# Optimization experiments

Measured on AMD Instinct MI355X. Metric: run time of the kernel, lower is better.

## Reference

```python
import jax, jax.numpy as jnp
import numpy as np

B, C, N, K, E = 8, 64, 4096, 16, 64
EPS = 1e-5


def _bn(h, gamma, beta, axes):
    # BatchNorm in training mode: stats over batch+spatial axes, per channel (dim 1)
    m = jnp.mean(h, axis=axes, keepdims=True)
    v = jnp.var(h, axis=axes, keepdims=True)
    shape = (1, -1) + (1,) * (h.ndim - 2)
    return gamma.reshape(shape) * (h - m) * jax.lax.rsqrt(v + EPS) + beta.reshape(shape)


def setup_inputs() -> dict:
    key = jax.random.key(0)
    ks = jax.random.split(key, 8)
    x = jax.random.normal(ks[0], (B, C, N), dtype=jnp.float32)
    idx = jax.random.randint(ks[1], (B, N, K), 0, N, dtype=jnp.int32)
    s1 = 1.0 / np.sqrt(C)
    s2 = 1.0 / np.sqrt(E)
    return {
        "x": x,
        "idx": idx,
        "W1": jax.random.normal(ks[2], (E, C), jnp.float32) * s1,
        "b1": jnp.zeros((E,), jnp.float32),
        "g1": jnp.ones((E,), jnp.float32),
        "be1": jnp.zeros((E,), jnp.float32),
        "W2": jax.random.normal(ks[3], (E, E), jnp.float32) * s2,
        "b2": jnp.zeros((E,), jnp.float32),
        "g2": jnp.ones((E,), jnp.float32),
        "be2": jnp.zeros((E,), jnp.float32),
        "W3": jax.random.normal(ks[4], (E, E), jnp.float32) * s2,
        "b3": jnp.zeros((E,), jnp.float32),
        "g3": jnp.ones((E,), jnp.float32),
        "be3": jnp.zeros((E,), jnp.float32),
    }


def reference(x, idx, W1, b1, g1, be1, W2, b2, g2, be2, W3, b3, g3, be3):
    # gather kNN neighbor features: x[b, :, idx[b]] -> (B, C, N, K)
    nn_feat = jax.vmap(lambda xb, ib: xb[:, ib])(x, idx)
    # edge features: neighbor - center
    h = nn_feat - x[..., None]                                   # (B, C, N, K)
    # Conv2DBlock: two 1x1 conv + BN + ReLU layers
    h = jnp.einsum('bcnk,oc->bonk', h, W1) + b1[:, None, None]
    h = jax.nn.relu(_bn(h, g1, be1, (0, 2, 3)))
    h = jnp.einsum('bcnk,oc->bonk', h, W2) + b2[:, None, None]
    h = jax.nn.relu(_bn(h, g2, be2, (0, 2, 3)))
    # max over neighbors
    h = jnp.max(h, axis=-1)                                      # (B, E, N)
    # Conv1DBlock: 1x1 conv + BN + ReLU
    h = jnp.einsum('bcn,oc->bon', h, W3) + b3[:, None]
    h = jax.nn.relu(_bn(h, g3, be3, (0, 2)))
    return h
```

## Files before the change

kernel.cpp:

```cpp
#include <hip/hip_runtime.h>

#define EPSBN 1e-5f
#define CNT1 524288.0f
#define CNT3 32768.0f
#define NREP 16

typedef short v8s __attribute__((ext_vector_type(8)));
typedef float v16f __attribute__((ext_vector_type(16)));

__device__ __forceinline__ unsigned short f2bf(float f) {
  union { float f; unsigned u; } v; v.f = f;
  unsigned u = v.u;
  u += 0x7fffu + ((u >> 16) & 1u);
  return (unsigned short)(u >> 16);
}
__device__ __forceinline__ unsigned pack2bf(float a, float b) {
  return (unsigned)f2bf(a) | ((unsigned)f2bf(b) << 16);
}
__device__ __forceinline__ float bflo(unsigned u) {
  union { unsigned u; float f; } v; v.u = u << 16; return v.f;
}
__device__ __forceinline__ float bfhi(unsigned u) {
  union { unsigned u; float f; } v; v.u = u & 0xffff0000u; return v.f;
}

__global__ __launch_bounds__(256) void prep(
    const float* __restrict__ x, const float* __restrict__ W1,
    const float* __restrict__ W2, const float* __restrict__ W3,
    unsigned short* __restrict__ y, unsigned short* __restrict__ Wbf) {
  int blk = blockIdx.x, t = threadIdx.x;
  if (blk >= 512) {
    int i = (blk - 512) * 256 + t;
    const float* src = (i < 4096) ? W2 : W3;
    Wbf[i] = f2bf(src[i & 4095]);
    return;
  }
  __shared__ unsigned short ldsX[64 * 72];
  int b = blk >> 6, n0 = (blk & 63) << 6;
  int tn = t & 63, cg = t >> 6;
#pragma unroll
  for (int i = 0; i < 16; ++i) {
    int c = cg * 16 + i;
    ldsX[tn * 72 + c] = f2bf(x[(((size_t)(b * 64 + c)) << 12) + n0 + tn]);
  }
  __syncthreads();
  int lane = t & 63, w = t >> 6;
  int l31 = lane & 31, lh = lane >> 5;
  int ot = w & 1, ph = w >> 1;
  int o = ot * 32 + l31;
  v16f acc;
#pragma unroll
  for (int i = 0; i < 16; ++i) acc[i] = 0.f;
#pragma unroll
  for (int ks = 0; ks < 4; ++ks) {
    const float* wrow = W1 + o * 64 + ks * 16 + lh * 8;
    float4 wa = *((const float4*)wrow);
    float4 wb = *((const float4*)(wrow + 4));
    v8s wf; unsigned* wu = (unsigned*)&wf;
    wu[0] = pack2bf(wa.x, wa.y); wu[1] = pack2bf(wa.z, wa.w);
    wu[2] = pack2bf(wb.x, wb.y); wu[3] = pack2bf(wb.z, wb.w);
    v8s af = *((const v8s*)&ldsX[(ph * 32 + l31) * 72 + ks * 16 + lh * 8]);
    acc = __builtin_amdgcn_mfma_f32_32x32x16_bf16(af, wf, acc, 0, 0, 0);
  }
#pragma unroll
  for (int i = 0; i < 16; ++i) {
    int row = (i & 3) + ((i >> 2) << 3) + (lh << 2);
    int pt = (b << 12) + n0 + ph * 32 + row;
    y[pt * 64 + o] = f2bf(acc[i]);
  }
}

__global__ __launch_bounds__(256) void p1_stats(
    const unsigned short* __restrict__ y, const int* __restrict__ idx,
    float* __restrict__ S1) {
  __shared__ float bs[64], bq[64];
  int t = threadIdx.x;
  if (t < 64) { bs[t] = 0.f; bq[t] = 0.f; }
  __syncthreads();
  int blk = blockIdx.x;
  int batch = blk & 7, bi = blk >> 3;
  int w = t >> 6, lane = t & 63;
  int ch = (lane & 7) << 3, eg = lane >> 3;
  int ebase = (batch << 16) + bi * 512 + w * 128;
  float ss[8], sq[8];
#pragma unroll
  for (int k = 0; k < 8; ++k) { ss[k] = 0.f; sq[k] = 0.f; }
  for (int it = 0; it < 16; ++it) {
    int p = ebase + it * 8 + eg;
    int j = idx[p];
    int site = p >> 4;
    uint4 uj = *((const uint4*)(y + (((size_t)((batch << 12) + j)) << 6) + ch));
    uint4 ui = *((const uint4*)(y + (((size_t)site) << 6) + ch));
    const unsigned* aj = (const unsigned*)&uj;
    const unsigned* ai = (const unsigned*)&ui;
#pragma unroll
    for (int d = 0; d < 4; ++d) {
      float d0 = bflo(aj[d]) - bflo(ai[d]);
      float d1 = bfhi(aj[d]) - bfhi(ai[d]);
      ss[2 * d] += d0; sq[2 * d] += d0 * d0;
      ss[2 * d + 1] += d1; sq[2 * d + 1] += d1 * d1;
    }
  }
#pragma unroll
  for (int k = 0; k < 8; ++k) {
    ss[k] += __shfl_xor(ss[k], 8);  sq[k] += __shfl_xor(sq[k], 8);
    ss[k] += __shfl_xor(ss[k], 16); sq[k] += __shfl_xor(sq[k], 16);
    ss[k] += __shfl_xor(ss[k], 32); sq[k] += __shfl_xor(sq[k], 32);
  }
  if (lane < 8) {
#pragma unroll
    for (int k = 0; k < 8; ++k) {
      atomicAdd(&bs[ch + k], ss[k]);
      atomicAdd(&bq[ch + k], sq[k]);
    }
  }
  __syncthreads();
  int rep = (blk >> 3) & (NREP - 1);
  if (t < 64) atomicAdd(&S1[rep * 128 + t], bs[t]);
  else if (t < 128) atomicAdd(&S1[rep * 128 + t], bq[t - 64]);
}

__global__ __launch_bounds__(256) void p1b_uv(
    const unsigned short* __restrict__ y,
    const float* __restrict__ g1, const float* __restrict__ be1,
    const float* __restrict__ S1,
    unsigned short* __restrict__ u, unsigned short* __restrict__ v) {
  __shared__ float lA[64], lC[64];
  int t = threadIdx.x;
  if (t < 64) {
    float s = 0.f, q = 0.f;
#pragma unroll
    for (int r = 0; r < NREP; ++r) { s += S1[r * 128 + t]; q += S1[r * 128 + 64 + t]; }
    float mean = s / CNT1;
    float var = q / CNT1 - mean * mean;
    float a = g1[t] * rsqrtf(var + EPSBN);
    lA[t] = a; lC[t] = be1[t] - mean * a;
  }
  __syncthreads();
  int pt = blockIdx.x * 64 + (t >> 2);
  int cq = (t & 3) << 4;
  const uint4* yp = (const uint4*)(y + (size_t)pt * 64 + cq);
  uint4 y0 = yp[0], y1 = yp[1];
  uint4 uo[2], vo[2];
  unsigned* up = (unsigned*)uo;
  unsigned* vp = (unsigned*)vo;
#pragma unroll
  for (int d = 0; d < 8; ++d) {
    unsigned yd = (d < 4) ? ((const unsigned*)&y0)[d] : ((const unsigned*)&y1)[d - 4];
    int c = cq + 2 * d;
    float f0 = bflo(yd), f1 = bfhi(yd);
    float a0 = lA[c], a1 = lA[c + 1];
    up[d] = pack2bf(f0 * a0 + lC[c], f1 * a1 + lC[c + 1]);
    vp[d] = pack2bf(f0 * a0, f1 * a1);
  }
  uint4* ud = (uint4*)(u + (size_t)pt * 64 + cq);
  uint4* vd = (uint4*)(v + (size_t)pt * 64 + cq);
  ud[0] = uo[0]; ud[1] = uo[1];
  vd[0] = vo[0]; vd[1] = vo[1];
}

__global__ __launch_bounds__(256) void p2_main(
    const unsigned short* __restrict__ u, const unsigned short* __restrict__ v,
    const int* __restrict__ idx, const unsigned short* __restrict__ Wb,
    unsigned short* __restrict__ mnb, unsigned short* __restrict__ mxb,
    float* __restrict__ S2) {
  __shared__ float bs[64], bq[64];
  int t = threadIdx.x;
  if (t < 64) { bs[t] = 0.f; bq[t] = 0.f; }
  __syncthreads();
  int blk = blockIdx.x;
  int batch = blk & 7, bi = blk >> 3;
  int w = t >> 6, lane = t & 63;
  int l31 = lane & 31, lh = lane >> 5;
  v8s w2[2][4];
#pragma unroll
  for (int s = 0; s < 2; ++s)
#pragma unroll
    for (int ks = 0; ks < 4; ++ks)
      w2[s][ks] = *((const v8s*)(Wb + (s * 32 + l31) * 64 + ks * 16 + lh * 8));
  float ss0 = 0.f, sq0 = 0.f, ss1 = 0.f, sq1 = 0.f;
#pragma unroll
  for (int it = 0; it < 2; ++it) {
    int tile = bi * 8 + w * 2 + it;
    int p = (batch << 16) + (tile << 5) + l31;
    int j = idx[p];
    int site = p >> 4;
    const unsigned short* ur = u + (((size_t)((batch << 12) + j)) << 6) + lh * 8;
    const unsigned short* vr = v + (((size_t)site) << 6) + lh * 8;
    v16f b0, b1;
#pragma unroll
    for (int i = 0; i < 16; ++i) { b0[i] = 0.f; b1[i] = 0.f; }
#pragma unroll
    for (int ks = 0; ks < 4; ++ks) {
      uint4 uu = *((const uint4*)(ur + ks * 16));
      uint4 vv = *((const uint4*)(vr + ks * 16));
      const unsigned* uw = (const unsigned*)&uu;
      const unsigned* vw = (const unsigned*)&vv;
      v8s af; unsigned* au = (unsigned*)&af;
#pragma unroll
      for (int d = 0; d < 4; ++d) {
        float e0 = fmaxf(bflo(uw[d]) - bflo(vw[d]), 0.f);
        float e1 = fmaxf(bfhi(uw[d]) - bfhi(vw[d]), 0.f);
        au[d] = pack2bf(e0, e1);
      }
      b0 = __builtin_amdgcn_mfma_f32_32x32x16_bf16(af, w2[0][ks], b0, 0, 0, 0);
      b1 = __builtin_amdgcn_mfma_f32_32x32x16_bf16(af, w2[1][ks], b1, 0, 0, 0);
    }
    float mx00 = b0[0], mn00 = b0[0], mx01 = b0[8], mn01 = b0[8];
    float mx10 = b1[0], mn10 = b1[0], mx11 = b1[8], mn11 = b1[8];
#pragma unroll
    for (int i = 0; i < 16; ++i) {
      ss0 += b0[i]; sq0 += b0[i] * b0[i];
      ss1 += b1[i]; sq1 += b1[i] * b1[i];
    }
#pragma unroll
    for (int i = 1; i < 8; ++i) {
      mx00 = fmaxf(mx00, b0[i]);     mn00 = fminf(mn00, b0[i]);
      mx01 = fmaxf(mx01, b0[8 + i]); mn01 = fminf(mn01, b0[8 + i]);
      mx10 = fmaxf(mx10, b1[i]);     mn10 = fminf(mn10, b1[i]);
      mx11 = fmaxf(mx11, b1[8 + i]); mn11 = fminf(mn11, b1[8 + i]);
    }
    mx00 = fmaxf(mx00, __shfl_xor(mx00, 32)); mn00 = fminf(mn00, __shfl_xor(mn00, 32));
    mx01 = fmaxf(mx01, __shfl_xor(mx01, 32)); mn01 = fminf(mn01, __shfl_xor(mn01, 32));
    mx10 = fmaxf(mx10, __shfl_xor(mx10, 32)); mn10 = fminf(mn10, __shfl_xor(mn10, 32));
    mx11 = fmaxf(mx11, __shfl_xor(mx11, 32)); mn11 = fminf(mn11, __shfl_xor(mn11, 32));
    int s2 = (batch << 12) + (tile << 1);
    if (lh == 0) {
      mnb[(size_t)(s2 + 0) * 64 + l31] = f2bf(mn00);
      mnb[(size_t)(s2 + 1) * 64 + l31] = f2bf(mn01);
      mnb[(size_t)(s2 + 0) * 64 + 32 + l31] = f2bf(mn10);
      mnb[(size_t)(s2 + 1) * 64 + 32 + l31] = f2bf(mn11);
    } else {
      mxb[(size_t)(s2 + 0) * 64 + l31] = f2bf(mx00);
      mxb[(size_t)(s2 + 1) * 64 + l31] = f2bf(mx01);
      mxb[(size_t)(s2 + 0) * 64 + 32 + l31] = f2bf(mx10);
      mxb[(size_t)(s2 + 1) * 64 + 32 + l31] = f2bf(mx11);
    }
  }
  ss0 += __shfl_xor(ss0, 32); sq0 += __shfl_xor(sq0, 32);
  ss1 += __shfl_xor(ss1, 32); sq1 += __shfl_xor(sq1, 32);
  if (lh == 0) {
    atomicAdd(&bs[l31], ss0); atomicAdd(&bq[l31], sq0);
    atomicAdd(&bs[32 + l31], ss1); atomicAdd(&bq[32 + l31], sq1);
  }
  __syncthreads();
  int rep = blk & (NREP - 1);
  if (t < 64) atomicAdd(&S2[rep * 128 + t], bs[t]);
  else if (t < 128) atomicAdd(&S2[rep * 128 + t], bq[t - 64]);
}

__global__ __launch_bounds__(256, 2) void p3_gemm3(
    const unsigned short* __restrict__ Wb,
    const unsigned short* __restrict__ mnb, const unsigned short* __restrict__ mxb,
    const float* __restrict__ g2, const float* __restrict__ be2,
    const float* __restrict__ S2, float* __restrict__ h3, float* __restrict__ S3) {
  __shared__ uint4 ldsA[64 * 9];
  __shared__ float bs[64], bq[64], lA[64], lC[64];
  int t = threadIdx.x;
  if (t < 64) {
    bs[t] = 0.f; bq[t] = 0.f;
    float s = 0.f, q = 0.f;
#pragma unroll
    for (int r = 0; r < NREP; ++r) { s += S2[r * 128 + t]; q += S2[r * 128 + 64 + t]; }
    float mean = s / CNT1;
    float var = q / CNT1 - mean * mean;
    float a = g2[t] * rsqrtf(var + EPSBN);
    lA[t] = a; lC[t] = be2[t] - mean * a;
  }
  __syncthreads();
  int lane = t & 63, wid = t >> 6;
  int rb = wid & 1, ctile = wid >> 1;
  int l31 = lane & 31, lh = lane >> 5;
  int o = ctile * 32 + l31;
  v8s wf[4];
#pragma unroll
  for (int ks = 0; ks < 4; ++ks)
    wf[ks] = *((const v8s*)(Wb + o * 64 + ks * 16 + lh * 8));
  int r = t >> 2, q = t & 3;
  int arow = rb * 32 + l31;
  int s0 = blockIdx.x << 6;
  {
    int site = s0 + r;
    const uint4* mnp = (const uint4*)(mnb + (size_t)site * 64 + q * 16);
    const uint4* mxp = (const uint4*)(mxb + (size_t)site * 64 + q * 16);
    uint4 m0 = mnp[0], m1 = mnp[1], x0 = mxp[0], x1 = mxp[1];
    uint4 ch2[2];
    unsigned* cu = (unsigned*)ch2;
#pragma unroll
    for (int d = 0; d < 8; ++d) {
      unsigned md = (d < 4) ? ((const unsigned*)&m0)[d] : ((const unsigned*)&m1)[d - 4];
      unsigned xd = (d < 4) ? ((const unsigned*)&x0)[d] : ((const unsigned*)&x1)[d - 4];
      int c = q * 16 + 2 * d;
      float a0 = lA[c], a1 = lA[c + 1];
      float s0v = (a0 > 0.f) ? bflo(xd) : bflo(md);
      float s1v = (a1 > 0.f) ? bfhi(xd) : bfhi(md);
      float v0 = fmaxf(a0 * s0v + lC[c], 0.f);
      float v1 = fmaxf(a1 * s1v + lC[c + 1], 0.f);
      cu[d] = pack2bf(v0, v1);
    }
    ldsA[r * 9 + q * 2 + 0] = ch2[0];
    ldsA[r * 9 + q * 2 + 1] = ch2[1];
  }
  __syncthreads();
  v16f acc;
#pragma unroll
  for (int i = 0; i < 16; ++i) acc[i] = 0.f;
#pragma unroll
  for (int ks = 0; ks < 4; ++ks) {
    v8s a = *((const v8s*)&ldsA[arow * 9 + ks * 2 + lh]);
    acc = __builtin_amdgcn_mfma_f32_32x32x16_bf16(a, wf[ks], acc, 0, 0, 0);
  }
  float ssum = 0.f, ssq = 0.f;
#pragma unroll
  for (int i = 0; i < 16; ++i) {
    float vv = acc[i];
    ssum += vv; ssq += vv * vv;
    int row = (i & 3) + ((i >> 2) << 3) + (lh << 2);
    h3[(((size_t)(s0 + rb * 32 + row)) << 6) + o] = vv;
  }
  ssum += __shfl_xor(ssum, 32);
  ssq += __shfl_xor(ssq, 32);
  if (lh == 0) { atomicAdd(&bs[o], ssum); atomicAdd(&bq[o], ssq); }
  __syncthreads();
  int rep = blockIdx.x & (NREP - 1);
  if (t < 64) atomicAdd(&S3[rep * 128 + t], bs[t]);
  else if (t < 128) atomicAdd(&S3[rep * 128 + t], bq[t - 64]);
}

__global__ void k4_out(const float* __restrict__ h3,
                       const float* __restrict__ g3, const float* __restrict__ be3,
                       float* __restrict__ out, const float* __restrict__ S3) {
  __shared__ float lA[64], lC[64];
  __shared__ float tile[64][65];
  int t = threadIdx.x;
  if (t < 64) {
    float s = 0.f, q = 0.f;
#pragma unroll
    for (int r = 0; r < NREP; ++r) { s += S3[r * 128 + t]; q += S3[r * 128 + 64 + t]; }
    float mean = s / CNT3;
    float var = q / CNT3 - mean * mean;
    float a = g3[t] * rsqrtf(var + EPSBN);
    lA[t] = a; lC[t] = be3[t] - mean * a;
  }
  __syncthreads();
  int blk = blockIdx.x;
  int b = blk >> 6, n0 = (blk & 63) << 6;
  int r = t >> 2, q = t & 3;
  const float4* hp = (const float4*)(h3 + (((size_t)((b << 12) + n0 + r)) << 6)) + q * 4;
#pragma unroll
  for (int ii = 0; ii < 4; ++ii) {
    float4 v = hp[ii];
    int c = q * 16 + ii * 4;
    tile[c + 0][r] = fmaxf(v.x * lA[c + 0] + lC[c + 0], 0.f);
    tile[c + 1][r] = fmaxf(v.y * lA[c + 1] + lC[c + 1], 0.f);
    tile[c + 2][r] = fmaxf(v.z * lA[c + 2] + lC[c + 2], 0.f);
    tile[c + 3][r] = fmaxf(v.w * lA[c + 3] + lC[c + 3], 0.f);
  }
  __syncthreads();
  int oo = t >> 2, seg = t & 3;
  float4* dst = (float4*)(out + (((size_t)(b * 64 + oo)) << 12) + n0 + seg * 16);
#pragma unroll
  for (int ii = 0; ii < 4; ++ii) {
    float4 v;
    v.x = tile[oo][seg * 16 + ii * 4 + 0];
    v.y = tile[oo][seg * 16 + ii * 4 + 1];
    v.z = tile[oo][seg * 16 + ii * 4 + 2];
    v.w = tile[oo][seg * 16 + ii * 4 + 3];
    dst[ii] = v;
  }
}

extern "C" void kernel_launch(void* const* d_in, const int* in_sizes, int n_in,
                              void* d_out, int out_size, void* d_ws, size_t ws_size,
                              hipStream_t stream) {
  const float* x = (const float*)d_in[0];
  const int* idx = (const int*)d_in[1];
  const float* W1 = (const float*)d_in[2];
  const float* g1 = (const float*)d_in[4];
  const float* be1 = (const float*)d_in[5];
  const float* W2 = (const float*)d_in[6];
  const float* g2 = (const float*)d_in[8];
  const float* be2 = (const float*)d_in[9];
  const float* W3 = (const float*)d_in[10];
  const float* g3 = (const float*)d_in[12];
  const float* be3 = (const float*)d_in[13];
  float* out = (float*)d_out;

  char* ws = (char*)d_ws;
  unsigned short* y   = (unsigned short*)ws;
  unsigned short* u   = (unsigned short*)(ws + (4u << 20));
  unsigned short* v   = (unsigned short*)(ws + (8u << 20));
  unsigned short* mnb = (unsigned short*)(ws + (12u << 20));
  unsigned short* mxb = (unsigned short*)(ws + (16u << 20));
  float* h3           = (float*)(ws + (20u << 20));
  unsigned short* Wbf = (unsigned short*)(ws + (28u << 20));
  float* stats        = (float*)(ws + (28u << 20) + (64u << 10));
  float* S1 = stats;
  float* S2 = stats + NREP * 128;
  float* S3 = stats + 2 * NREP * 128;

  hipMemsetAsync(stats, 0, 3 * NREP * 128 * sizeof(float), stream);
  prep<<<544, 256, 0, stream>>>(x, W1, W2, W3, y, Wbf);
  p1_stats<<<1024, 256, 0, stream>>>(y, idx, S1);
  p1b_uv<<<512, 256, 0, stream>>>(y, g1, be1, S1, u, v);
  p2_main<<<2048, 256, 0, stream>>>(u, v, idx, Wbf, mnb, mxb, S2);
  p3_gemm3<<<512, 256, 0, stream>>>(Wbf + 4096, mnb, mxb, g2, be2, S2, h3, S3);
  k4_out<<<512, 256, 0, stream>>>(h3, g3, be3, out, S3);
}
```

Measured before the change: 147.4 us.

## Fuse BN1 affine into edge GEMM kernel and drop u/v intermediates

Removes the p1b_uv kernel, which wrote two bf16 tensors u and v. p2_main now gathers y directly and applies the BN1 scale and shift per element from shared memory. The W2/W3 bf16 conversion moves from prep into the consuming kernels, which convert the fp32 weights in registers. p2_main now processes 8 tiles per wave with a 4x smaller grid, trading one launch and about 8 MB of traffic for extra per-element FMAs and lower parallelism. Numerics shift slightly because the affine is now applied to the bf16 difference instead of rounding u and v separately.

```diff
diff --git a/kernel.cpp b/kernel.cpp
--- a/kernel.cpp
+++ b/kernel.cpp
@@ -26,16 +26,9 @@
 
 __global__ __launch_bounds__(256) void prep(
     const float* __restrict__ x, const float* __restrict__ W1,
-    const float* __restrict__ W2, const float* __restrict__ W3,
-    unsigned short* __restrict__ y, unsigned short* __restrict__ Wbf) {
+    unsigned short* __restrict__ y) {
+  __shared__ unsigned short ldsX[64 * 72];
   int blk = blockIdx.x, t = threadIdx.x;
-  if (blk >= 512) {
-    int i = (blk - 512) * 256 + t;
-    const float* src = (i < 4096) ? W2 : W3;
-    Wbf[i] = f2bf(src[i & 4095]);
-    return;
-  }
-  __shared__ unsigned short ldsX[64 * 72];
   int b = blk >> 6, n0 = (blk & 63) << 6;
   int tn = t & 63, cg = t >> 6;
 #pragma unroll
@@ -120,14 +113,19 @@
   else if (t < 128) atomicAdd(&S1[rep * 128 + t], bq[t - 64]);
 }
 
-__global__ __launch_bounds__(256) void p1b_uv(
-    const unsigned short* __restrict__ y,
+__global__ __launch_bounds__(256) void p2_main(
+    const unsigned short* __restrict__ y, const int* __restrict__ idx,
+    const float* __restrict__ W2f,
     const float* __restrict__ g1, const float* __restrict__ be1,
     const float* __restrict__ S1,
-    unsigned short* __restrict__ u, unsigned short* __restrict__ v) {
-  __shared__ float lA[64], lC[64];
+    unsigned short* __restrict__ mnb, unsigned short* __restrict__ mxb,
+    float* __restrict__ S2) {
+  __shared__ float bs[64], bq[64];
+  __shared__ __align__(16) float lA[64];
+  __shared__ __align__(16) float lC[64];
   int t = threadIdx.x;
   if (t < 64) {
+    bs[t] = 0.f; bq[t] = 0.f;
     float s = 0.f, q = 0.f;
 #pragma unroll
     for (int r = 0; r < NREP; ++r) { s += S1[r * 128 + t]; q += S1[r * 128 + 64 + t]; }
@@ -137,37 +135,6 @@
     lA[t] = a; lC[t] = be1[t] - mean * a;
   }
   __syncthreads();
-  int pt = blockIdx.x * 64 + (t >> 2);
-  int cq = (t & 3) << 4;
-  const uint4* yp = (const uint4*)(y + (size_t)pt * 64 + cq);
-  uint4 y0 = yp[0], y1 = yp[1];
-  uint4 uo[2], vo[2];
-  unsigned* up = (unsigned*)uo;
-  unsigned* vp = (unsigned*)vo;
-#pragma unroll
-  for (int d = 0; d < 8; ++d) {
-    unsigned yd = (d < 4) ? ((const unsigned*)&y0)[d] : ((const unsigned*)&y1)[d - 4];
-    int c = cq + 2 * d;
-    float f0 = bflo(yd), f1 = bfhi(yd);
-    float a0 = lA[c], a1 = lA[c + 1];
-    up[d] = pack2bf(f0 * a0 + lC[c], f1 * a1 + lC[c + 1]);
-    vp[d] = pack2bf(f0 * a0, f1 * a1);
-  }
-  uint4* ud = (uint4*)(u + (size_t)pt * 64 + cq);
-  uint4* vd = (uint4*)(v + (size_t)pt * 64 + cq);
-  ud[0] = uo[0]; ud[1] = uo[1];
-  vd[0] = vo[0]; vd[1] = vo[1];
-}
-
-__global__ __launch_bounds__(256) void p2_main(
-    const unsigned short* __restrict__ u, const unsigned short* __restrict__ v,
-    const int* __restrict__ idx, const unsigned short* __restrict__ Wb,
-    unsigned short* __restrict__ mnb, unsigned short* __restrict__ mxb,
-    float* __restrict__ S2) {
-  __shared__ float bs[64], bq[64];
-  int t = threadIdx.x;
-  if (t < 64) { bs[t] = 0.f; bq[t] = 0.f; }
-  __syncthreads();
   int blk = blockIdx.x;
   int batch = blk & 7, bi = blk >> 3;
   int w = t >> 6, lane = t & 63;
@@ -176,31 +143,42 @@
 #pragma unroll
   for (int s = 0; s < 2; ++s)
 #pragma unroll
-    for (int ks = 0; ks < 4; ++ks)
-      w2[s][ks] = *((const v8s*)(Wb + (s * 32 + l31) * 64 + ks * 16 + lh * 8));
+    for (int ks = 0; ks < 4; ++ks) {
+      const float* wr = W2f + (s * 32 + l31) * 64 + ks * 16 + lh * 8;
+      float4 wa = *((const float4*)wr);
+      float4 wb = *((const float4*)(wr + 4));
+      unsigned* wu = (unsigned*)&w2[s][ks];
+      wu[0] = pack2bf(wa.x, wa.y); wu[1] = pack2bf(wa.z, wa.w);
+      wu[2] = pack2bf(wb.x, wb.y); wu[3] = pack2bf(wb.z, wb.w);
+    }
   float ss0 = 0.f, sq0 = 0.f, ss1 = 0.f, sq1 = 0.f;
-#pragma unroll
-  for (int it = 0; it < 2; ++it) {
-    int tile = bi * 8 + w * 2 + it;
+  for (int it = 0; it < 8; ++it) {
+    int tile = bi * 32 + w * 8 + it;
     int p = (batch << 16) + (tile << 5) + l31;
     int j = idx[p];
     int site = p >> 4;
-    const unsigned short* ur = u + (((size_t)((batch << 12) + j)) << 6) + lh * 8;
-    const unsigned short* vr = v + (((size_t)site) << 6) + lh * 8;
+    const unsigned short* yj = y + (((size_t)((batch << 12) + j)) << 6) + lh * 8;
+    const unsigned short* yi = y + (((size_t)site) << 6) + lh * 8;
     v16f b0, b1;
 #pragma unroll
     for (int i = 0; i < 16; ++i) { b0[i] = 0.f; b1[i] = 0.f; }
 #pragma unroll
     for (int ks = 0; ks < 4; ++ks) {
-      uint4 uu = *((const uint4*)(ur + ks * 16));
-      uint4 vv = *((const uint4*)(vr + ks * 16));
-      const unsigned* uw = (const unsigned*)&uu;
-      const unsigned* vw = (const unsigned*)&vv;
+      uint4 uj = *((const uint4*)(yj + ks * 16));
+      uint4 ui = *((const uint4*)(yi + ks * 16));
+      float4 a0 = *((const float4*)&lA[ks * 16 + lh * 8]);
+      float4 a1 = *((const float4*)&lA[ks * 16 + lh * 8 + 4]);
+      float4 c0 = *((const float4*)&lC[ks * 16 + lh * 8]);
+      float4 c1 = *((const float4*)&lC[ks * 16 + lh * 8 + 4]);
+      float av[8] = {a0.x, a0.y, a0.z, a0.w, a1.x, a1.y, a1.z, a1.w};
+      float cv[8] = {c0.x, c0.y, c0.z, c0.w, c1.x, c1.y, c1.z, c1.w};
+      const unsigned* jw = (const unsigned*)&uj;
+      const unsigned* iw = (const unsigned*)&ui;
       v8s af; unsigned* au = (unsigned*)&af;
 #pragma unroll
       for (int d = 0; d < 4; ++d) {
-        float e0 = fmaxf(bflo(uw[d]) - bflo(vw[d]), 0.f);
-        float e1 = fmaxf(bfhi(uw[d]) - bfhi(vw[d]), 0.f);
+        float e0 = fmaxf((bflo(jw[d]) - bflo(iw[d])) * av[2 * d] + cv[2 * d], 0.f);
+        float e1 = fmaxf((bfhi(jw[d]) - bfhi(iw[d])) * av[2 * d + 1] + cv[2 * d + 1], 0.f);
         au[d] = pack2bf(e0, e1);
       }
       b0 = __builtin_amdgcn_mfma_f32_32x32x16_bf16(af, w2[0][ks], b0, 0, 0, 0);
@@ -250,7 +228,7 @@
 }
 
 __global__ __launch_bounds__(256, 2) void p3_gemm3(
-    const unsigned short* __restrict__ Wb,
+    const float* __restrict__ W3f,
     const unsigned short* __restrict__ mnb, const unsigned short* __restrict__ mxb,
     const float* __restrict__ g2, const float* __restrict__ be2,
     const float* __restrict__ S2, float* __restrict__ h3, float* __restrict__ S3) {
@@ -274,8 +252,14 @@
   int o = ctile * 32 + l31;
   v8s wf[4];
 #pragma unroll
-  for (int ks = 0; ks < 4; ++ks)
-    wf[ks] = *((const v8s*)(Wb + o * 64 + ks * 16 + lh * 8));
+  for (int ks = 0; ks < 4; ++ks) {
+    const float* wr = W3f + o * 64 + ks * 16 + lh * 8;
+    float4 wa = *((const float4*)wr);
+    float4 wb = *((const float4*)(wr + 4));
+    unsigned* wu = (unsigned*)&wf[ks];
+    wu[0] = pack2bf(wa.x, wa.y); wu[1] = pack2bf(wa.z, wa.w);
+    wu[2] = pack2bf(wb.x, wb.y); wu[3] = pack2bf(wb.z, wb.w);
+  }
   int r = t >> 2, q = t & 3;
   int arow = rb * 32 + l31;
   int s0 = blockIdx.x << 6;
@@ -388,22 +372,18 @@
 
   char* ws = (char*)d_ws;
   unsigned short* y   = (unsigned short*)ws;
-  unsigned short* u   = (unsigned short*)(ws + (4u << 20));
-  unsigned short* v   = (unsigned short*)(ws + (8u << 20));
-  unsigned short* mnb = (unsigned short*)(ws + (12u << 20));
-  unsigned short* mxb = (unsigned short*)(ws + (16u << 20));
-  float* h3           = (float*)(ws + (20u << 20));
-  unsigned short* Wbf = (unsigned short*)(ws + (28u << 20));
-  float* stats        = (float*)(ws + (28u << 20) + (64u << 10));
+  unsigned short* mnb = (unsigned short*)(ws + (4u << 20));
+  unsigned short* mxb = (unsigned short*)(ws + (8u << 20));
+  float* h3           = (float*)(ws + (12u << 20));
+  float* stats        = (float*)(ws + (20u << 20));
   float* S1 = stats;
   float* S2 = stats + NREP * 128;
   float* S3 = stats + 2 * NREP * 128;
 
   hipMemsetAsync(stats, 0, 3 * NREP * 128 * sizeof(float), stream);
-  prep<<<544, 256, 0, stream>>>(x, W1, W2, W3, y, Wbf);
+  prep<<<512, 256, 0, stream>>>(x, W1, y);
   p1_stats<<<1024, 256, 0, stream>>>(y, idx, S1);
-  p1b_uv<<<512, 256, 0, stream>>>(y, g1, be1, S1, u, v);
-  p2_main<<<2048, 256, 0, stream>>>(u, v, idx, Wbf, mnb, mxb, S2);
-  p3_gemm3<<<512, 256, 0, stream>>>(Wbf + 4096, mnb, mxb, g2, be2, S2, h3, S3);
+  p2_main<<<512, 256, 0, stream>>>(y, idx, W2, g1, be1, S1, mnb, mxb, S2);
+  p3_gemm3<<<512, 256, 0, stream>>>(W3, mnb, mxb, g2, be2, S2, h3, S3);
   k4_out<<<512, 256, 0, stream>>>(h3, g3, be3, out, S3);
 }
```

Result: faster. 140.9 us (-4.4%).
